# Kernel tuning notes

Measured on AMD Instinct MI355X. Metric: run time of the kernel, lower is better.

The kernel has to match this reference:

```python
import jax, jax.numpy as jnp
import numpy as np

DROPOUT_RATE = 0.25
STRIDE = 5  # must be odd


def setup_inputs() -> dict:
    key = jax.random.key(0)
    k1, k2 = jax.random.split(key)
    b, c, h, w = 4, 256, 64, 64
    x = jax.random.normal(k1, (b, c, h, w), dtype=jnp.float32)
    # uniform randoms underlying the dropout mask on the expanded grid
    rand_vals = jax.random.uniform(k2, (h * STRIDE, w * STRIDE), dtype=jnp.float32)
    return {"x": x, "rand_vals": rand_vals}


def reference(x, rand_vals):
    s = STRIDE
    s2 = s // 2
    rate = DROPOUT_RATE
    b, c, h, w = x.shape
    # zero-pad spatial dims by s//2 (ZeroPad2d)
    xp = jnp.pad(x, ((0, 0), (0, 0), (s2, s2), (s2, s2)))
    # x_new[:, :, i*s+p, j*s+q] = xp[:, :, i+p, j+q]  -> single fused gather
    idx_h = (jnp.arange(h)[:, None] + jnp.arange(s)[None, :]).reshape(h * s)  # [h*s]
    idx_w = (jnp.arange(w)[:, None] + jnp.arange(s)[None, :]).reshape(w * s)  # [w*s]
    x_new = xp[:, :, idx_h[:, None], idx_w[None, :]]  # [b, c, h*s, w*s]
    # dropout mask with forced keep at each patch center (s2 + i*s, s2 + j*s)
    mask = rand_vals > rate
    mask = mask.at[s2::s, s2::s].set(True)
    return x_new * mask.astype(x_new.dtype) / (1.0 - rate)
```

## Files before the change

### kernel.cpp

```cpp
#include <hip/hip_runtime.h>
#include <stdint.h>


#define KEEP_SCALE (1.0f / 0.75f)

typedef float f32x4 __attribute__((ext_vector_type(4)));

__global__ __launch_bounds__(256) void build_mask_kernel(
    const float* __restrict__ rv,
    uint32_t* __restrict__ mask)
{
    int w = blockIdx.x * 256 + threadIdx.x;
    if (w >= 3200) return;
    int oh  = w / 10;
    int ow0 = (w - oh * 10) * 32;
    int qh = oh / 5, rh = oh - qh * 5;
    int ih = qh + rh - 2;
    bool hok = ((unsigned)ih < 64u);
    bool hc  = (rh == 2);
    const float* rp = rv + oh * 320 + ow0;
    uint32_t m = 0;
    #pragma unroll
    for (int b = 0; b < 32; ++b) {
        int ow = ow0 + b;
        int q = ow / 5, r = ow - q * 5;
        int iw = q + r - 2;
        bool keep = ((rp[b] > 0.25f) || (hc && (r == 2)))
                    && hok && ((unsigned)iw < 64u);
        m |= (uint32_t)keep << b;
    }
    mask[w] = m;
}

__global__ __launch_bounds__(320) void expand_cps_dropout_kernel(
    const float* __restrict__ x,
    const uint32_t* __restrict__ mask,
    float* __restrict__ out)
{
    __shared__ float    xs[12 * 64];
    __shared__ uint32_t ms[400];

    const int t  = threadIdx.x;
    const int g  = blockIdx.x;
    const int bc = blockIdx.y;

    int s0 = 8 * g - 2;
    s0 = s0 < 0 ? 0 : (s0 > 52 ? 52 : s0);

    if (t < 192) {
        const float* xsrc = x + (size_t)bc * 4096 + s0 * 64;
        __builtin_amdgcn_global_load_lds(
            (const __attribute__((address_space(1))) void*)(xsrc + t * 4),
            (__attribute__((address_space(3))) void*)(xs + (t & ~63) * 4),
            16, 0, 0);
    } else if (t < 292) {
        int i = t - 192;
        const uint32_t* msrc = mask + g * 400;
        __builtin_amdgcn_global_load_lds(
            (const __attribute__((address_space(1))) void*)(msrc + i * 4),
            (__attribute__((address_space(3))) void*)(ms + (i & ~63) * 4),
            16, 0, 0);
    }
    __syncthreads();

    const int ow4 = t % 80;
    const int ohL = t / 80;
    const int ow  = ow4 * 4;

    int xoffb[4];
    #pragma unroll
    for (int k = 0; k < 4; ++k) {
        int o = ow + k;
        int q = o / 5, r = o - q * 5;
        int iw = q + r - 2;
        iw = iw < 0 ? 0 : (iw > 63 ? 63 : iw);
        xoffb[k] = iw * 4;
    }
    const int msh = (ow4 & 7) * 4;
    const uint32_t* msp = ms + ohL * 10 + (ow4 >> 3);
    const char* xsb = (const char*)xs;

    const int ohbase = g * 40 + ohL;
    float* op = out + (size_t)bc * 102400 + (size_t)ohbase * 320 + ow;

    #pragma unroll
    for (int j = 0; j < 10; ++j) {
        int oh = ohbase + 4 * j;
        int q = oh / 5, r = oh - q * 5;
        int ih = q + r - 2;
        ih = ih < s0 ? s0 : (ih > s0 + 11 ? s0 + 11 : ih);
        const char* xr = xsb + (ih - s0) * 256;
        uint32_t mb = msp[j * 40] >> msh;

        f32x4 o;
        o.x = (mb & 1u) ? *(const float*)(xr + xoffb[0]) * KEEP_SCALE : 0.0f;
        o.y = (mb & 2u) ? *(const float*)(xr + xoffb[1]) * KEEP_SCALE : 0.0f;
        o.z = (mb & 4u) ? *(const float*)(xr + xoffb[2]) * KEEP_SCALE : 0.0f;
        o.w = (mb & 8u) ? *(const float*)(xr + xoffb[3]) * KEEP_SCALE : 0.0f;
        *reinterpret_cast<f32x4*>(op + (size_t)(4 * j) * 320) = o;
    }
}

extern "C" void kernel_launch(void* const* d_in, const int* in_sizes, int n_in,
                              void* d_out, int out_size, void* d_ws, size_t ws_size,
                              hipStream_t stream) {
    const float* x  = (const float*)d_in[0];
    const float* rv = (const float*)d_in[1];
    float* out      = (float*)d_out;
    uint32_t* mask  = (uint32_t*)d_ws;

    hipLaunchKernelGGL(build_mask_kernel, dim3(13), dim3(256), 0, stream, rv, mask);

    dim3 block(320);
    dim3 grid(8, 1024);
    hipLaunchKernelGGL(expand_cps_dropout_kernel, grid, block, 0, stream,
                       x, mask, out);
}
```

Measured before the change: 91.66 us.

## Process four batch-channel planes per block with double-buffered LDS input prefetch

```diff
diff --git a/kernel.cpp b/kernel.cpp
--- a/kernel.cpp
+++ b/kernel.cpp
@@ -37,21 +37,22 @@
     const uint32_t* __restrict__ mask,
     float* __restrict__ out)
 {
-    __shared__ float    xs[12 * 64];
-    __shared__ uint32_t ms[400];
+    __shared__ __align__(16) float    xs[2][12 * 64];
+    __shared__ __align__(16) uint32_t ms[400];
 
-    const int t  = threadIdx.x;
-    const int g  = blockIdx.x;
-    const int bc = blockIdx.y;
+    const int t   = threadIdx.x;
+    const int b   = blockIdx.x;
+    const int g   = b & 7;
+    const int bc0 = b >> 3;
 
     int s0 = 8 * g - 2;
     s0 = s0 < 0 ? 0 : (s0 > 52 ? 52 : s0);
 
+    const float* xsrc0 = x + (size_t)bc0 * 4096 + s0 * 64;
     if (t < 192) {
-        const float* xsrc = x + (size_t)bc * 4096 + s0 * 64;
         __builtin_amdgcn_global_load_lds(
-            (const __attribute__((address_space(1))) void*)(xsrc + t * 4),
-            (__attribute__((address_space(3))) void*)(xs + (t & ~63) * 4),
+            (const __attribute__((address_space(1))) void*)(xsrc0 + t * 4),
+            (__attribute__((address_space(3))) void*)(&xs[0][0] + (t & ~63) * 4),
             16, 0, 0);
     } else if (t < 292) {
         int i = t - 192;
@@ -61,43 +62,67 @@
             (__attribute__((address_space(3))) void*)(ms + (i & ~63) * 4),
             16, 0, 0);
     }
-    __syncthreads();
 
     const int ow4 = t % 80;
     const int ohL = t / 80;
     const int ow  = ow4 * 4;
+    const int msh = (ow4 & 7) * 4;
+    const int mwi = ow4 >> 3;
 
-    int xoffb[4];
+    int xoffB[4];
     #pragma unroll
     for (int k = 0; k < 4; ++k) {
         int o = ow + k;
         int q = o / 5, r = o - q * 5;
         int iw = q + r - 2;
         iw = iw < 0 ? 0 : (iw > 63 ? 63 : iw);
-        xoffb[k] = iw * 4;
+        xoffB[k] = iw * 4;
     }
-    const int msh = (ow4 & 7) * 4;
-    const uint32_t* msp = ms + ohL * 10 + (ow4 >> 3);
-    const char* xsb = (const char*)xs;
+    int rowB[10];
+    #pragma unroll
+    for (int j = 0; j < 10; ++j) {
+        int oh = g * 40 + ohL + 4 * j;
+        int q = oh / 5, r = oh - q * 5;
+        int ihrel = q + r - 2 - s0;
+        ihrel = ihrel < 0 ? 0 : (ihrel > 11 ? 11 : ihrel);
+        rowB[j] = ihrel * 256;
+    }
+    float* outb = out + (size_t)bc0 * 102400 + (size_t)(g * 40 + ohL) * 320 + ow;
 
-    const int ohbase = g * 40 + ohL;
-    float* op = out + (size_t)bc * 102400 + (size_t)ohbase * 320 + ow;
+    __syncthreads();
+
+    uint32_t mb[10];
+    #pragma unroll
+    for (int j = 0; j < 10; ++j)
+        mb[j] = ms[(ohL + 4 * j) * 10 + mwi] >> msh;
 
     #pragma unroll
-    for (int j = 0; j < 10; ++j) {
-        int oh = ohbase + 4 * j;
-        int q = oh / 5, r = oh - q * 5;
-        int ih = q + r - 2;
-        ih = ih < s0 ? s0 : (ih > s0 + 11 ? s0 + 11 : ih);
-        const char* xr = xsb + (ih - s0) * 256;
-        uint32_t mb = msp[j * 40] >> msh;
+    for (int it = 0; it < 4; ++it) {
+        if (it < 3 && t < 192) {
+            const float* xsrcn =
+                x + (size_t)(bc0 + 256 * (it + 1)) * 4096 + s0 * 64;
+            __builtin_amdgcn_global_load_lds(
+                (const __attribute__((address_space(1))) void*)(xsrcn + t * 4),
+                (__attribute__((address_space(3))) void*)(&xs[(it + 1) & 1][0] + (t & ~63) * 4),
+                16, 0, 0);
+        }
 
-        f32x4 o;
-        o.x = (mb & 1u) ? *(const float*)(xr + xoffb[0]) * KEEP_SCALE : 0.0f;
-        o.y = (mb & 2u) ? *(const float*)(xr + xoffb[1]) * KEEP_SCALE : 0.0f;
-        o.z = (mb & 4u) ? *(const float*)(xr + xoffb[2]) * KEEP_SCALE : 0.0f;
-        o.w = (mb & 8u) ? *(const float*)(xr + xoffb[3]) * KEEP_SCALE : 0.0f;
-        *reinterpret_cast<f32x4*>(op + (size_t)(4 * j) * 320) = o;
+        const char* xb = (const char*)&xs[it & 1][0];
+        float* op = outb + (size_t)it * 256 * 102400;
+
+        #pragma unroll
+        for (int j = 0; j < 10; ++j) {
+            const char* xr = xb + rowB[j];
+            uint32_t m = mb[j];
+            f32x4 o;
+            o.x = (m & 1u) ? *(const float*)(xr + xoffB[0]) * KEEP_SCALE : 0.0f;
+            o.y = (m & 2u) ? *(const float*)(xr + xoffB[1]) * KEEP_SCALE : 0.0f;
+            o.z = (m & 4u) ? *(const float*)(xr + xoffB[2]) * KEEP_SCALE : 0.0f;
+            o.w = (m & 8u) ? *(const float*)(xr + xoffB[3]) * KEEP_SCALE : 0.0f;
+            *reinterpret_cast<f32x4*>(op + (size_t)(4 * j) * 320) = o;
+        }
+
+        if (it < 3) __syncthreads();
     }
 }
 
@@ -112,7 +137,7 @@
     hipLaunchKernelGGL(build_mask_kernel, dim3(13), dim3(256), 0, stream, rv, mask);
 
     dim3 block(320);
-    dim3 grid(8, 1024);
+    dim3 grid(2048);
     hipLaunchKernelGGL(expand_cps_dropout_kernel, grid, block, 0, stream,
                        x, mask, out);
 }
```

Result: slower. 98.05 us (+7.0%).

## Retile expand kernel into 16-row blocks with 256 threads and precomputed offsets

Applied to the files above, without the earlier changes.

```diff
diff --git a/kernel.cpp b/kernel.cpp
--- a/kernel.cpp
+++ b/kernel.cpp
@@ -32,72 +32,87 @@
     mask[w] = m;
 }
 
-__global__ __launch_bounds__(320) void expand_cps_dropout_kernel(
+__global__ __launch_bounds__(256) void expand_cps_dropout_kernel(
     const float* __restrict__ x,
     const uint32_t* __restrict__ mask,
     float* __restrict__ out)
 {
-    __shared__ float    xs[12 * 64];
-    __shared__ uint32_t ms[400];
+    __shared__ __align__(16) float    xs[8 * 64];
+    __shared__ __align__(16) uint32_t ms[160];
 
     const int t  = threadIdx.x;
-    const int g  = blockIdx.x;
-    const int bc = blockIdx.y;
+    const int b  = blockIdx.x;
+    const int bc = b / 20;
+    const int rg = b - bc * 20;
 
-    int s0 = 8 * g - 2;
-    s0 = s0 < 0 ? 0 : (s0 > 52 ? 52 : s0);
+    const int a = 16 * rg;
+    int s0 = a / 5 - 2;
+    s0 = s0 < 0 ? 0 : (s0 > 56 ? 56 : s0);
 
-    if (t < 192) {
+    if (t < 128) {
         const float* xsrc = x + (size_t)bc * 4096 + s0 * 64;
         __builtin_amdgcn_global_load_lds(
             (const __attribute__((address_space(1))) void*)(xsrc + t * 4),
             (__attribute__((address_space(3))) void*)(xs + (t & ~63) * 4),
             16, 0, 0);
-    } else if (t < 292) {
-        int i = t - 192;
-        const uint32_t* msrc = mask + g * 400;
+    } else if (t < 168) {
+        int i = t - 128;
+        const uint32_t* msrc = mask + rg * 160;
         __builtin_amdgcn_global_load_lds(
             (const __attribute__((address_space(1))) void*)(msrc + i * 4),
             (__attribute__((address_space(3))) void*)(ms + (i & ~63) * 4),
             16, 0, 0);
     }
+
+    int      xoffB[5][4];
+    int      rowB[5];
+    int      soffF[5];
+    int      midx[5];
+    uint32_t msh_[5];
+    #pragma unroll
+    for (int ji = 0; ji < 5; ++ji) {
+        int f  = t + 256 * ji;
+        int r0 = f / 80;
+        int o4 = f - r0 * 80;
+        int ow = o4 * 4;
+        soffF[ji] = r0 * 320 + ow;
+        msh_[ji]  = (uint32_t)((o4 & 7) * 4);
+        midx[ji]  = r0 * 10 + (o4 >> 3);
+        int oh = a + r0;
+        int q = oh / 5, r = oh - q * 5;
+        int ihrel = q + r - 2 - s0;
+        ihrel = ihrel < 0 ? 0 : (ihrel > 7 ? 7 : ihrel);
+        rowB[ji] = ihrel * 256;
+        #pragma unroll
+        for (int k = 0; k < 4; ++k) {
+            int o = ow + k;
+            int qq = o / 5, rr = o - qq * 5;
+            int iw = qq + rr - 2;
+            iw = iw < 0 ? 0 : (iw > 63 ? 63 : iw);
+            xoffB[ji][k] = iw * 4;
+        }
+    }
+
     __syncthreads();
 
-    const int ow4 = t % 80;
-    const int ohL = t / 80;
-    const int ow  = ow4 * 4;
+    uint32_t mb[5];
+    #pragma unroll
+    for (int ji = 0; ji < 5; ++ji)
+        mb[ji] = ms[midx[ji]] >> msh_[ji];
 
-    int xoffb[4];
-    #pragma unroll
-    for (int k = 0; k < 4; ++k) {
-        int o = ow + k;
-        int q = o / 5, r = o - q * 5;
-        int iw = q + r - 2;
-        iw = iw < 0 ? 0 : (iw > 63 ? 63 : iw);
-        xoffb[k] = iw * 4;
-    }
-    const int msh = (ow4 & 7) * 4;
-    const uint32_t* msp = ms + ohL * 10 + (ow4 >> 3);
+    float* ob = out + (size_t)b * 5120;
     const char* xsb = (const char*)xs;
 
-    const int ohbase = g * 40 + ohL;
-    float* op = out + (size_t)bc * 102400 + (size_t)ohbase * 320 + ow;
-
     #pragma unroll
-    for (int j = 0; j < 10; ++j) {
-        int oh = ohbase + 4 * j;
-        int q = oh / 5, r = oh - q * 5;
-        int ih = q + r - 2;
-        ih = ih < s0 ? s0 : (ih > s0 + 11 ? s0 + 11 : ih);
-        const char* xr = xsb + (ih - s0) * 256;
-        uint32_t mb = msp[j * 40] >> msh;
-
+    for (int ji = 0; ji < 5; ++ji) {
+        const char* xr = xsb + rowB[ji];
+        uint32_t m = mb[ji];
         f32x4 o;
-        o.x = (mb & 1u) ? *(const float*)(xr + xoffb[0]) * KEEP_SCALE : 0.0f;
-        o.y = (mb & 2u) ? *(const float*)(xr + xoffb[1]) * KEEP_SCALE : 0.0f;
-        o.z = (mb & 4u) ? *(const float*)(xr + xoffb[2]) * KEEP_SCALE : 0.0f;
-        o.w = (mb & 8u) ? *(const float*)(xr + xoffb[3]) * KEEP_SCALE : 0.0f;
-        *reinterpret_cast<f32x4*>(op + (size_t)(4 * j) * 320) = o;
+        o.x = (m & 1u) ? *(const float*)(xr + xoffB[ji][0]) * KEEP_SCALE : 0.0f;
+        o.y = (m & 2u) ? *(const float*)(xr + xoffB[ji][1]) * KEEP_SCALE : 0.0f;
+        o.z = (m & 4u) ? *(const float*)(xr + xoffB[ji][2]) * KEEP_SCALE : 0.0f;
+        o.w = (m & 8u) ? *(const float*)(xr + xoffB[ji][3]) * KEEP_SCALE : 0.0f;
+        *reinterpret_cast<f32x4*>(ob + soffF[ji]) = o;
     }
 }
 
@@ -111,8 +126,8 @@
 
     hipLaunchKernelGGL(build_mask_kernel, dim3(13), dim3(256), 0, stream, rv, mask);
 
-    dim3 block(320);
-    dim3 grid(8, 1024);
+    dim3 block(256);
+    dim3 grid(20480);
     hipLaunchKernelGGL(expand_cps_dropout_kernel, grid, block, 0, stream,
                        x, mask, out);
 }
```

Result: faster. 87.15 us (-4.9%).
